# Optimization experiments

Hardware: AMD Instinct MI355X
Metric: run time of the kernel (lower is better)

The kernel has to match this reference:

```python
import jax, jax.numpy as jnp
import numpy as np

SEQ_LEN = 12
EMB = 64        # embedding_dim
H = 128         # dec_h_dim
MLP = 1024      # mlp_dim
Z = 32          # z_dim
ZX = MLP + Z    # 1056, width of cat([enc_h_feat, z])
B = 32768


def setup_inputs() -> dict:
    key = jax.random.key(0)
    ks = jax.random.split(key, 16)
    s = 0.05  # weight scale to keep the recurrence stable
    return {
        "last_pos": jax.random.normal(ks[0], (B, 2), jnp.float32),
        "last_pos_rel": jax.random.normal(ks[1], (B, 2), jnp.float32),
        "enc_h_feat": jax.random.normal(ks[2], (B, MLP), jnp.float32),
        "z": jax.random.normal(ks[3], (B, Z), jnp.float32),
        "seq_start_end": jnp.zeros((1, 2), jnp.int64),
        # LSTM params (PyTorch layout: gates ordered i,f,g,o along rows)
        "W_ih": jax.random.normal(ks[4], (4 * H, ZX + EMB), jnp.float32) * s,
        "W_hh": jax.random.normal(ks[5], (4 * H, H), jnp.float32) * s,
        "b_ih": jax.random.normal(ks[6], (4 * H,), jnp.float32) * s,
        "b_hh": jax.random.normal(ks[7], (4 * H,), jnp.float32) * s,
        # mlp: Linear(ZX->MLP), ReLU, Linear(MLP->H), ReLU
        "W1": jax.random.normal(ks[8], (MLP, ZX), jnp.float32) * s,
        "b1": jax.random.normal(ks[9], (MLP,), jnp.float32) * s,
        "W2": jax.random.normal(ks[10], (H, MLP), jnp.float32) * s,
        "b2": jax.random.normal(ks[11], (H,), jnp.float32) * s,
        # spatial_embedding: Linear(2 -> EMB)
        "W_sp": jax.random.normal(ks[12], (EMB, 2), jnp.float32) * s,
        "b_sp": jax.random.normal(ks[13], (EMB,), jnp.float32) * s,
        # hidden2pos: Linear(H -> 2)
        "W_hp": jax.random.normal(ks[14], (2, H), jnp.float32) * s,
        "b_hp": jax.random.normal(ks[15], (2,), jnp.float32) * s,
    }


def _decode(last_pos, last_pos_rel, enc_h_feat, z,
            W_ih, W_hh, b_ih, b_hh, W1, b1, W2, b2, W_sp, b_sp, W_hp, b_hp):
    # initial decoder input from last relative position
    dec_inp = last_pos_rel @ W_sp.T + b_sp                     # [B, EMB]
    zx = jnp.concatenate([enc_h_feat, z], axis=1)              # [B, ZX]
    h = jax.nn.relu(jax.nn.relu(zx @ W1.T + b1) @ W2.T + b2)   # [B, H]
    c = jnp.zeros_like(h)
    # zx is constant across steps: precompute its gate contribution + biases
    W_zx, W_emb = W_ih[:, :ZX], W_ih[:, ZX:]
    zx_proj = zx @ W_zx.T + b_ih + b_hh                        # [B, 4H]

    def step(carry, _):
        h, c, last_pos, dec_inp = carry
        gates = zx_proj + dec_inp @ W_emb.T + h @ W_hh.T       # [B, 4H]
        i, f, g, o = jnp.split(gates, 4, axis=1)
        c = jax.nn.sigmoid(f) * c + jax.nn.sigmoid(i) * jnp.tanh(g)
        h = jax.nn.sigmoid(o) * jnp.tanh(c)
        rel_pos = h @ W_hp.T + b_hp                            # [B, 2]
        last_pos = rel_pos + last_pos
        dec_inp = rel_pos @ W_sp.T + b_sp
        return (h, c, last_pos, dec_inp), rel_pos

    _, pred = jax.lax.scan(step, (h, c, last_pos, dec_inp), None, length=SEQ_LEN)
    return pred  # [SEQ_LEN, B, 2]


def reference(last_pos, last_pos_rel, enc_h_feat, z, seq_start_end,
              W_ih, W_hh, b_ih, b_hh, W1, b1, W2, b2, W_sp, b_sp, W_hp, b_hp):
    # seq_start_end is unused by the original forward
    return _decode(last_pos, last_pos_rel, enc_h_feat, z,
                   W_ih, W_hh, b_ih, b_hh, W1, b1, W2, b2, W_sp, b_sp, W_hp, b_hp)
```

## Files before the change

### kernel.cpp

```cpp
#include <hip/hip_runtime.h>

#define BATCH   32768
#define SEQLEN  12
#define EMB     64
#define H       128
#define MLP     1024
#define Z       32
#define ZX      1056
#define KP      1088
#define NG      512

typedef _Float16 f16x8 __attribute__((ext_vector_type(8)));
typedef float    f32x4 __attribute__((ext_vector_type(4)));

#define S_WCAT_OFF   0u
#define S_W2H_OFF    3244032u
#define S_WHHF_OFF   3506176u
#define S_WC_OFF     3637248u
#define S_BIAS2_OFF  3641344u
#define S_T1_OFF     3643392u
#define S_GP_OFF     70752256u
#define S_H0_OFF     137861120u
#define B_WCAT_OFF   0u
#define B_W2H_OFF    3342336u
#define B_WHHF_OFF   3604480u
#define B_WC_OFF     3735552u
#define B_BIAS2_OFF  3739648u
#define B_T1_OFF     3741696u
#define B_GP_OFF     70850560u
#define B_H0_OFF     137959424u
#define B_ZX16_OFF   146348032u
#define B_TOTAL      217651200ull

__device__ __forceinline__ float sigf(float x) {
    return __builtin_amdgcn_rcpf(1.0f + __expf(-x));
}
__device__ __forceinline__ float tanhfast(float x) {
    return 2.0f * __builtin_amdgcn_rcpf(1.0f + __expf(-2.0f * x)) - 1.0f;
}

__device__ __forceinline__ void gload16(const void* g, void* l) {
    __builtin_amdgcn_global_load_lds(
        (const __attribute__((address_space(1))) unsigned int*)(unsigned long long)(uintptr_t)g,
        (__attribute__((address_space(3))) unsigned int*)(unsigned int)(uintptr_t)l,
        16, 0, 0);
}

__global__ __launch_bounds__(256) void prep_kernel(
    const float* __restrict__ W_ih, const float* __restrict__ W_hh_in,
    const float* __restrict__ b_ih, const float* __restrict__ b_hh,
    const float* __restrict__ W1,   const float* __restrict__ W2,
    const float* __restrict__ W_sp, const float* __restrict__ b_sp,
    const float* __restrict__ W_hp, int cs,
    _Float16* __restrict__ wcat, _Float16* __restrict__ w2h,
    _Float16* __restrict__ whhf, float* __restrict__ wc, float* __restrict__ bias2)
{
    const int bid = blockIdx.x;
    const int tid = threadIdx.x;
    if (bid < 1536) {
        const float* src = (bid < 1024) ? (W1 + (size_t)bid * ZX)
                                        : (W_ih + (size_t)(bid - 1024) * 1120);
        _Float16* dst = wcat + (size_t)bid * cs;
        for (int k = tid; k < cs; k += 256)
            dst[k] = (k < ZX) ? (_Float16)src[k] : (_Float16)0.f;
    } else if (bid < 1664) {
        const int n = bid - 1536;
        for (int k = tid; k < MLP; k += 256)
            w2h[n * MLP + k] = (_Float16)W2[n * MLP + k];
    } else if (bid < 1920) {
        const int n = (bid - 1664) * 2 + (tid >> 7);
        const int k = tid & 127;
        float wc0 = 0.f, wc1 = 0.f;
        for (int e = 0; e < EMB; ++e) {
            const float we = W_ih[(size_t)n * 1120 + ZX + e];
            wc0 += we * W_sp[e * 2];
            wc1 += we * W_sp[e * 2 + 1];
        }
        whhf[n * H + k] = (_Float16)(W_hh_in[n * H + k] + wc0 * W_hp[k] + wc1 * W_hp[H + k]);
    } else {
        const int t = (bid - 1920) * 256 + tid;
        if (t < 1024) {
            const int n = t >> 1, j = t & 1;
            float s = 0.f;
            for (int e = 0; e < EMB; ++e)
                s += W_ih[(size_t)n * 1120 + ZX + e] * W_sp[e * 2 + j];
            wc[t] = s;
        } else if (t < 1536) {
            const int n = t - 1024;
            float s = b_ih[n] + b_hh[n];
            for (int e = 0; e < EMB; ++e)
                s += W_ih[(size_t)n * 1120 + ZX + e] * b_sp[e];
            bias2[n] = s;
        }
    }
}

__global__ __launch_bounds__(256) void zxcast_kernel(
    const float* __restrict__ enc, const float* __restrict__ zin,
    _Float16* __restrict__ zx16)
{
    const int gid = blockIdx.x * 256 + threadIdx.x;
    if (gid < 4194304) {
        const int row = gid >> 7, cw = gid & 127;
        const float4* s = (const float4*)(enc + (size_t)row * MLP + cw * 8);
        const float4 f0 = s[0], f1 = s[1];
        f16x8 v = {(_Float16)f0.x, (_Float16)f0.y, (_Float16)f0.z, (_Float16)f0.w,
                   (_Float16)f1.x, (_Float16)f1.y, (_Float16)f1.z, (_Float16)f1.w};
        *(f16x8*)(zx16 + (size_t)row * KP + cw * 8) = v;
    } else if (gid < 4325376) {
        const int g2 = gid - 4194304;
        const int row = g2 >> 2, cw = g2 & 3;
        const float4* s = (const float4*)(zin + (size_t)row * Z + cw * 8);
        const float4 f0 = s[0], f1 = s[1];
        f16x8 v = {(_Float16)f0.x, (_Float16)f0.y, (_Float16)f0.z, (_Float16)f0.w,
                   (_Float16)f1.x, (_Float16)f1.y, (_Float16)f1.z, (_Float16)f1.w};
        *(f16x8*)(zx16 + (size_t)row * KP + MLP + cw * 8) = v;
    } else {
        const int g2 = gid - 4325376;
        const int row = g2 >> 2, cw = g2 & 3;
        f16x8 v = {};
        *(f16x8*)(zx16 + (size_t)row * KP + ZX + cw * 8) = v;
    }
}

__global__ __launch_bounds__(256) void gemm1_big_kernel(
    const _Float16* __restrict__ zx16, const _Float16* __restrict__ wcat,
    const float* __restrict__ bias1, const float* __restrict__ bias2g,
    _Float16* __restrict__ t1, float* __restrict__ gperm)
{
    __shared__ _Float16 s_a[128 * 64];
    __shared__ _Float16 s_b[128 * 64];

    const int tid = threadIdx.x;
    const int b = blockIdx.x;
    const int x = b & 7, s = b >> 3;
    const int mt = x * 32 + s / 12;
    const int bn = s % 12;
    const int m0 = mt * 128;

    const int lane = tid & 63, wv = tid >> 6;
    const int wm = wv >> 1, wn = wv & 1;
    const int l15 = lane & 15, q = lane >> 4;

    const int rowS = tid >> 3;
    const int chS  = (tid & 7) ^ ((tid >> 3) & 7);

    f32x4 acc[4][4] = {};

    for (int kt = 0; kt < 17; ++kt) {
        __syncthreads();
        #pragma unroll
        for (int i = 0; i < 4; ++i)
            gload16(zx16 + (size_t)(m0 + i * 32 + rowS) * KP + kt * 64 + chS * 8,
                    s_a + i * 2048 + wv * 512);
        #pragma unroll
        for (int i = 0; i < 4; ++i)
            gload16(wcat + (size_t)(bn * 128 + i * 32 + rowS) * KP + kt * 64 + chS * 8,
                    s_b + i * 2048 + wv * 512);
        __syncthreads();

        #pragma unroll
        for (int kt2 = 0; kt2 < 2; ++kt2) {
            f16x8 af[4];
            #pragma unroll
            for (int im = 0; im < 4; ++im) {
                const int row = wm * 64 + im * 16 + l15;
                const int ph  = (kt2 * 4 + q) ^ (l15 & 7);
                af[im] = *(const f16x8*)(s_a + row * 64 + ph * 8);
            }
            #pragma unroll
            for (int in_ = 0; in_ < 4; ++in_) {
                const int row = wn * 64 + in_ * 16 + l15;
                const int ph  = (kt2 * 4 + q) ^ (l15 & 7);
                const f16x8 bf = *(const f16x8*)(s_b + row * 64 + ph * 8);
                #pragma unroll
                for (int im = 0; im < 4; ++im)
                    acc[im][in_] = __builtin_amdgcn_mfma_f32_16x16x32_f16(af[im], bf, acc[im][in_], 0, 0, 0);
            }
        }
    }

    if (bn < 8) {
        #pragma unroll
        for (int im = 0; im < 4; ++im)
            #pragma unroll
            for (int in_ = 0; in_ < 4; ++in_) {
                const int n = bn * 128 + wn * 64 + in_ * 16 + l15;
                const float bb = bias1[n];
                #pragma unroll
                for (int r = 0; r < 4; ++r) {
                    const int m = m0 + wm * 64 + im * 16 + q * 4 + r;
                    float v = acc[im][in_][r] + bb;
                    v = v > 0.f ? v : 0.f;
                    t1[(size_t)m * MLP + n] = (_Float16)v;
                }
            }
    } else {
        #pragma unroll
        for (int im = 0; im < 4; ++im)
            #pragma unroll
            for (int in_ = 0; in_ < 4; ++in_) {
                const int n = (bn - 8) * 128 + wn * 64 + in_ * 16 + l15;
                const float bb = bias2g[n];
                const int m4 = (m0 + wm * 64 + im * 16 + q * 4) >> 2;
                float4 v;
                v.x = acc[im][in_][0] + bb;
                v.y = acc[im][in_][1] + bb;
                v.z = acc[im][in_][2] + bb;
                v.w = acc[im][in_][3] + bb;
                *(float4*)(gperm + ((size_t)m4 * NG + n) * 4) = v;
            }
    }
}

__global__ __launch_bounds__(256) void gemm1_small_kernel(
    const float* __restrict__ enc, const float* __restrict__ zin,
    const _Float16* __restrict__ wcat,
    const float* __restrict__ bias1, const float* __restrict__ bias2g,
    _Float16* __restrict__ t1, float* __restrict__ gperm)
{
    __shared__ float    s_a[128 * 32];
    __shared__ _Float16 s_b[128 * 32];

    const int tid = threadIdx.x;
    const int b = blockIdx.x;
    const int x = b & 7, s = b >> 3;
    const int mt = x * 32 + s / 12;
    const int bn = s % 12;
    const int m0 = mt * 128;

    const int lane = tid & 63, wv = tid >> 6;
    const int wm = wv >> 1, wn = wv & 1;
    const int l15 = lane & 15, q = lane >> 4;

    const int rowA = tid >> 3;
    const int chA  = (tid & 7) ^ ((tid >> 3) & 7);
    const int rowB = tid >> 2;
    const int chB  = (tid & 3) ^ ((tid >> 3) & 3);

    const int ca0 = (2 * q) ^ (l15 & 7);
    const int cb  = q ^ ((l15 >> 1) & 3);

    f32x4 acc[4][4] = {};

    for (int kt = 0; kt < 33; ++kt) {
        const float* abase;
        size_t astride;
        if (kt < 32) { abase = enc + (size_t)m0 * MLP + kt * 32; astride = MLP; }
        else         { abase = zin + (size_t)m0 * Z;             astride = Z;   }

        __syncthreads();
        #pragma unroll
        for (int i = 0; i < 4; ++i)
            gload16(abase + (size_t)(i * 32 + rowA) * astride + chA * 4,
                    s_a + i * 1024 + wv * 256);
        #pragma unroll
        for (int i = 0; i < 2; ++i)
            gload16(wcat + (size_t)(bn * 128 + i * 64 + rowB) * ZX + kt * 32 + chB * 8,
                    s_b + i * 2048 + wv * 512);
        __syncthreads();

        f16x8 af[4];
        #pragma unroll
        for (int im = 0; im < 4; ++im) {
            const float* ap = s_a + (wm * 64 + im * 16 + l15) * 32;
            const float4 f0 = *(const float4*)(ap + ca0 * 4);
            const float4 f1 = *(const float4*)(ap + (ca0 ^ 1) * 4);
            af[im] = f16x8{(_Float16)f0.x, (_Float16)f0.y, (_Float16)f0.z, (_Float16)f0.w,
                           (_Float16)f1.x, (_Float16)f1.y, (_Float16)f1.z, (_Float16)f1.w};
        }
        #pragma unroll
        for (int in_ = 0; in_ < 4; ++in_) {
            const f16x8 bf = *(const f16x8*)(s_b + (wn * 64 + in_ * 16 + l15) * 32 + cb * 8);
            #pragma unroll
            for (int im = 0; im < 4; ++im)
                acc[im][in_] = __builtin_amdgcn_mfma_f32_16x16x32_f16(af[im], bf, acc[im][in_], 0, 0, 0);
        }
    }

    if (bn < 8) {
        #pragma unroll
        for (int im = 0; im < 4; ++im)
            #pragma unroll
            for (int in_ = 0; in_ < 4; ++in_) {
                const int n = bn * 128 + wn * 64 + in_ * 16 + l15;
                const float bb = bias1[n];
                #pragma unroll
                for (int r = 0; r < 4; ++r) {
                    const int m = m0 + wm * 64 + im * 16 + q * 4 + r;
                    float v = acc[im][in_][r] + bb;
                    v = v > 0.f ? v : 0.f;
                    t1[(size_t)m * MLP + n] = (_Float16)v;
                }
            }
    } else {
        #pragma unroll
        for (int im = 0; im < 4; ++im)
            #pragma unroll
            for (int in_ = 0; in_ < 4; ++in_) {
                const int n = (bn - 8) * 128 + wn * 64 + in_ * 16 + l15;
                const float bb = bias2g[n];
                const int m4 = (m0 + wm * 64 + im * 16 + q * 4) >> 2;
                float4 v;
                v.x = acc[im][in_][0] + bb;
                v.y = acc[im][in_][1] + bb;
                v.z = acc[im][in_][2] + bb;
                v.w = acc[im][in_][3] + bb;
                *(float4*)(gperm + ((size_t)m4 * NG + n) * 4) = v;
            }
    }
}

__global__ __launch_bounds__(256) void gemm2_kernel(
    const _Float16* __restrict__ t1, const _Float16* __restrict__ w2h,
    const float* __restrict__ b2, _Float16* __restrict__ h0buf)
{
    __shared__ _Float16 s_a[64 * 32];
    __shared__ _Float16 s_b[128 * 32];

    const int tid = threadIdx.x;
    const int m0  = blockIdx.x * 64;
    const int lane = tid & 63, wv = tid >> 6;
    const int l15 = lane & 15, q = lane >> 4;

    const int rowS = tid >> 2;
    const int chS  = ((tid & 3) ^ (tid >> 2) ^ (tid >> 4)) & 3;
    const int phF  = (q ^ l15 ^ (l15 >> 2)) & 3;

    f32x4 acc[4][2] = {};

    for (int kt = 0; kt < 32; ++kt) {
        __syncthreads();
        gload16(t1 + (size_t)(m0 + rowS) * MLP + kt * 32 + chS * 8,
                s_a + wv * 512);
        #pragma unroll
        for (int i = 0; i < 2; ++i) {
            const int row = i * 64 + rowS;
            const int c   = ((tid & 3) ^ row ^ (row >> 2)) & 3;
            gload16(w2h + (size_t)row * MLP + kt * 32 + c * 8,
                    s_b + i * 2048 + wv * 512);
        }
        __syncthreads();

        f16x8 af[4];
        #pragma unroll
        for (int im = 0; im < 4; ++im)
            af[im] = *(const f16x8*)(s_a + (im * 16 + l15) * 32 + phF * 8);
        #pragma unroll
        for (int in_ = 0; in_ < 2; ++in_) {
            const f16x8 bf = *(const f16x8*)(s_b + (wv * 32 + in_ * 16 + l15) * 32 + phF * 8);
            #pragma unroll
            for (int im = 0; im < 4; ++im)
                acc[im][in_] = __builtin_amdgcn_mfma_f32_16x16x32_f16(af[im], bf, acc[im][in_], 0, 0, 0);
        }
    }

    #pragma unroll
    for (int im = 0; im < 4; ++im)
        #pragma unroll
        for (int in_ = 0; in_ < 2; ++in_) {
            const int n = wv * 32 + in_ * 16 + l15;
            const float bb = b2[n];
            #pragma unroll
            for (int r = 0; r < 4; ++r) {
                const int m = m0 + im * 16 + q * 4 + r;
                float v = acc[im][in_][r] + bb;
                v = v > 0.f ? v : 0.f;
                h0buf[(size_t)m * H + n] = (_Float16)v;
            }
        }
}

__global__ __launch_bounds__(512) void recur_kernel(
    const float* __restrict__ gperm, const _Float16* __restrict__ h0buf,
    const _Float16* __restrict__ whhf, const float* __restrict__ wc,
    const float* __restrict__ whp, const float* __restrict__ bhp,
    const float* __restrict__ lpr, float* __restrict__ out)
{
    __shared__ _Float16 s_whh[512 * 136];
    __shared__ _Float16 s_h[64 * 136];
    __shared__ float    s_p[128];
    __shared__ float    s_wc[1024];
    __shared__ float    s_whp[256];
    __shared__ float    s_bhp[2];

    const int tid = threadIdx.x;
    const int m0  = blockIdx.x * 64;
    const int lane = tid & 63, w = tid >> 6;
    const int l15 = lane & 15, q = lane >> 4;

    #pragma unroll
    for (int i = 0; i < 16; ++i) {
        const int cid = tid + i * 512;
        const int row = cid >> 4, ch = cid & 15;
        *(uint4*)(s_whh + row * 136 + ch * 8) = *(const uint4*)(whhf + row * H + ch * 8);
    }
    if (tid < 256) *(float4*)(s_wc + tid * 4)  = *(const float4*)(wc + tid * 4);
    if (tid < 64)  *(float4*)(s_whp + tid * 4) = *(const float4*)(whp + tid * 4);
    if (tid < 2)   s_bhp[tid] = bhp[tid];
    if (tid < 128) s_p[tid] = lpr[(size_t)m0 * 2 + tid];
    {
        const int row = tid >> 3, ch = tid & 7;
        *(uint4*)(s_h + row * 136 + ch * 16)     = *(const uint4*)(h0buf + (size_t)(m0 + row) * H + ch * 16);
        *(uint4*)(s_h + row * 136 + ch * 16 + 8) = *(const uint4*)(h0buf + (size_t)(m0 + row) * H + ch * 16 + 8);
    }

    f32x4 gb[4][4];
    #pragma unroll
    for (int im = 0; im < 4; ++im) {
        const int m4 = (m0 >> 2) + im * 4 + q;
        #pragma unroll
        for (int g = 0; g < 4; ++g) {
            const float4 v = *(const float4*)(gperm + ((size_t)m4 * NG + g * H + w * 16 + l15) * 4);
            gb[im][g] = f32x4{v.x, v.y, v.z, v.w};
        }
    }

    f32x4 cst[4] = {};

    __syncthreads();

    {
        const int part = tid & 3;
        const int j    = (tid >> 2) & 1;
        const int row  = tid >> 3;
        float sum = 0.f;
        #pragma unroll
        for (int u = 0; u < 4; ++u) {
            const f16x8 hv = *(const f16x8*)(s_h + row * 136 + part * 32 + u * 8);
            const float4* wp = (const float4*)(s_whp + j * H + part * 32 + u * 8);
            const float4 w0 = wp[0], w1 = wp[1];
            sum += (float)hv[0] * w0.x + (float)hv[1] * w0.y + (float)hv[2] * w0.z + (float)hv[3] * w0.w
                 + (float)hv[4] * w1.x + (float)hv[5] * w1.y + (float)hv[6] * w1.z + (float)hv[7] * w1.w;
        }
        sum += __shfl_down(sum, 2, 64);
        sum += __shfl_down(sum, 1, 64);
        if (part == 0) s_p[row * 2 + j] -= sum;
    }
    __syncthreads();

    float wc0[4], wc1[4], cg[4];
    #pragma unroll
    for (int g = 0; g < 4; ++g) {
        const int n = g * H + w * 16 + l15;
        wc0[g] = s_wc[n * 2];
        wc1[g] = s_wc[n * 2 + 1];
        cg[g]  = wc0[g] * s_bhp[0] + wc1[g] * s_bhp[1];
    }
    #pragma unroll
    for (int im = 0; im < 4; ++im)
        #pragma unroll
        for (int r = 0; r < 4; ++r) {
            const int mrow = im * 16 + q * 4 + r;
            const float pa = s_p[mrow * 2], pb = s_p[mrow * 2 + 1];
            #pragma unroll
            for (int g = 0; g < 4; ++g)
                gb[im][g][r] += pa * wc0[g] + pb * wc1[g];
        }

    for (int t = 0; t < SEQLEN; ++t) {
        f32x4 acc[4][4];
        #pragma unroll
        for (int kt = 0; kt < 4; ++kt) {
            f16x8 af[4];
            #pragma unroll
            for (int im = 0; im < 4; ++im)
                af[im] = *(const f16x8*)(s_h + (im * 16 + l15) * 136 + kt * 32 + q * 8);
            #pragma unroll
            for (int g = 0; g < 4; ++g) {
                const f16x8 bf = *(const f16x8*)(s_whh + (g * H + w * 16 + l15) * 136 + kt * 32 + q * 8);
                #pragma unroll
                for (int im = 0; im < 4; ++im)
                    acc[im][g] = __builtin_amdgcn_mfma_f32_16x16x32_f16(
                        af[im], bf, (kt == 0) ? gb[im][g] : acc[im][g], 0, 0, 0);
            }
        }
        __syncthreads();

        #pragma unroll
        for (int im = 0; im < 4; ++im) {
            #pragma unroll
            for (int r = 0; r < 4; ++r) {
                const int mrow = im * 16 + q * 4 + r;
                const float cc = sigf(acc[im][1][r]) * cst[im][r]
                               + sigf(acc[im][0][r]) * tanhfast(acc[im][2][r]);
                cst[im][r] = cc;
                const float hh = sigf(acc[im][3][r]) * tanhfast(cc);
                s_h[mrow * 136 + w * 16 + l15] = (_Float16)hh;
            }
        }
        if (t == 0) {
            #pragma unroll
            for (int im = 0; im < 4; ++im)
                #pragma unroll
                for (int r = 0; r < 4; ++r) {
                    const int mrow = im * 16 + q * 4 + r;
                    const float pa = s_p[mrow * 2], pb = s_p[mrow * 2 + 1];
                    #pragma unroll
                    for (int g = 0; g < 4; ++g)
                        gb[im][g][r] += cg[g] - (pa * wc0[g] + pb * wc1[g]);
                }
        }
        __syncthreads();

        {
            const int part = tid & 3;
            const int j    = (tid >> 2) & 1;
            const int row  = tid >> 3;
            float sum = 0.f;
            #pragma unroll
            for (int u = 0; u < 4; ++u) {
                const f16x8 hv = *(const f16x8*)(s_h + row * 136 + part * 32 + u * 8);
                const float4* wp = (const float4*)(s_whp + j * H + part * 32 + u * 8);
                const float4 w0 = wp[0], w1 = wp[1];
                sum += (float)hv[0] * w0.x + (float)hv[1] * w0.y + (float)hv[2] * w0.z + (float)hv[3] * w0.w
                     + (float)hv[4] * w1.x + (float)hv[5] * w1.y + (float)hv[6] * w1.z + (float)hv[7] * w1.w;
            }
            sum += __shfl_down(sum, 2, 64);
            sum += __shfl_down(sum, 1, 64);
            if (part == 0)
                out[(size_t)t * (BATCH * 2) + (size_t)(m0 + row) * 2 + j] = sum + s_bhp[j];
        }
    }
}

extern "C" void kernel_launch(void* const* d_in, const int* in_sizes, int n_in,
                              void* d_out, int out_size, void* d_ws, size_t ws_size,
                              hipStream_t stream)
{
    const float* last_pos_rel = (const float*)d_in[1];
    const float* enc          = (const float*)d_in[2];
    const float* zin          = (const float*)d_in[3];
    const float* W_ih         = (const float*)d_in[5];
    const float* W_hh         = (const float*)d_in[6];
    const float* b_ih         = (const float*)d_in[7];
    const float* b_hh         = (const float*)d_in[8];
    const float* W1           = (const float*)d_in[9];
    const float* b1           = (const float*)d_in[10];
    const float* W2           = (const float*)d_in[11];
    const float* b2           = (const float*)d_in[12];
    const float* W_sp         = (const float*)d_in[13];
    const float* b_sp         = (const float*)d_in[14];
    const float* W_hp         = (const float*)d_in[15];
    const float* b_hp         = (const float*)d_in[16];
    float* out = (float*)d_out;

    char* ws = (char*)d_ws;
    const bool big = (ws_size >= B_TOTAL);

    _Float16* wcat  = (_Float16*)(ws + (big ? B_WCAT_OFF  : S_WCAT_OFF));
    _Float16* w2h   = (_Float16*)(ws + (big ? B_W2H_OFF   : S_W2H_OFF));
    _Float16* whhf  = (_Float16*)(ws + (big ? B_WHHF_OFF  : S_WHHF_OFF));
    float*    wc    = (float*)(ws + (big ? B_WC_OFF    : S_WC_OFF));
    float*    bias2 = (float*)(ws + (big ? B_BIAS2_OFF : S_BIAS2_OFF));
    _Float16* t1    = (_Float16*)(ws + (big ? B_T1_OFF : S_T1_OFF));
    float*    gperm = (float*)(ws + (big ? B_GP_OFF : S_GP_OFF));
    _Float16* h0b   = (_Float16*)(ws + (big ? B_H0_OFF : S_H0_OFF));
    _Float16* zx16  = (_Float16*)(ws + B_ZX16_OFF);

    prep_kernel<<<dim3(1926), 256, 0, stream>>>(W_ih, W_hh, b_ih, b_hh, W1, W2, W_sp, b_sp,
                                                W_hp, big ? KP : ZX, wcat, w2h, whhf, wc, bias2);
    if (big) {
        zxcast_kernel<<<dim3(17408), 256, 0, stream>>>(enc, zin, zx16);
        gemm1_big_kernel<<<dim3(3072), 256, 0, stream>>>(zx16, wcat, b1, bias2, t1, gperm);
    } else {
        gemm1_small_kernel<<<dim3(3072), 256, 0, stream>>>(enc, zin, wcat, b1, bias2, t1, gperm);
    }
    gemm2_kernel<<<dim3(512), 256, 0, stream>>>(t1, w2h, b2, h0b);
    recur_kernel<<<dim3(512), 512, 0, stream>>>(gperm, h0b, whhf, wc, W_hp, b_hp,
                                                last_pos_rel, out);
}
```

Baseline: 530.6 us.

## Keep recurrent weights in registers and vectorize weight conversion in prep

The recurrence kernel no longer stages the 512x128 fp16 W_hh matrix in shared memory. Each wave instead loads its own MFMA B-fragments into registers once, and launch bounds request two blocks per CU. This cuts LDS use from about 150KB to about 25KB, which permits more resident blocks and removes the per-step LDS reads of weights, at the cost of 64 extra VGPRs per thread. The prep kernel's fp32-to-fp16 weight conversion is also vectorized to 8-wide loads and stores.

```diff
diff --git a/kernel.cpp b/kernel.cpp
--- a/kernel.cpp
+++ b/kernel.cpp
@@ -61,12 +61,26 @@
         const float* src = (bid < 1024) ? (W1 + (size_t)bid * ZX)
                                         : (W_ih + (size_t)(bid - 1024) * 1120);
         _Float16* dst = wcat + (size_t)bid * cs;
-        for (int k = tid; k < cs; k += 256)
-            dst[k] = (k < ZX) ? (_Float16)src[k] : (_Float16)0.f;
+        const int nch = cs >> 3;
+        for (int c = tid; c < nch; c += 256) {
+            f16x8 v = {};
+            if (c < 132) {
+                const float4 f0 = *(const float4*)(src + c * 8);
+                const float4 f1 = *(const float4*)(src + c * 8 + 4);
+                v = f16x8{(_Float16)f0.x, (_Float16)f0.y, (_Float16)f0.z, (_Float16)f0.w,
+                          (_Float16)f1.x, (_Float16)f1.y, (_Float16)f1.z, (_Float16)f1.w};
+            }
+            *(f16x8*)(dst + c * 8) = v;
+        }
     } else if (bid < 1664) {
         const int n = bid - 1536;
-        for (int k = tid; k < MLP; k += 256)
-            w2h[n * MLP + k] = (_Float16)W2[n * MLP + k];
+        for (int c = tid; c < 128; c += 256) {
+            const float4 f0 = *(const float4*)(W2 + (size_t)n * MLP + c * 8);
+            const float4 f1 = *(const float4*)(W2 + (size_t)n * MLP + c * 8 + 4);
+            f16x8 v = {(_Float16)f0.x, (_Float16)f0.y, (_Float16)f0.z, (_Float16)f0.w,
+                       (_Float16)f1.x, (_Float16)f1.y, (_Float16)f1.z, (_Float16)f1.w};
+            *(f16x8*)(w2h + (size_t)n * MLP + c * 8) = v;
+        }
     } else if (bid < 1920) {
         const int n = (bid - 1664) * 2 + (tid >> 7);
         const int k = tid & 127;
@@ -371,13 +385,12 @@
         }
 }
 
-__global__ __launch_bounds__(512) void recur_kernel(
+__global__ __launch_bounds__(512, 2) void recur_kernel(
     const float* __restrict__ gperm, const _Float16* __restrict__ h0buf,
     const _Float16* __restrict__ whhf, const float* __restrict__ wc,
     const float* __restrict__ whp, const float* __restrict__ bhp,
     const float* __restrict__ lpr, float* __restrict__ out)
 {
-    __shared__ _Float16 s_whh[512 * 136];
     __shared__ _Float16 s_h[64 * 136];
     __shared__ float    s_p[128];
     __shared__ float    s_wc[1024];
@@ -389,12 +402,13 @@
     const int lane = tid & 63, w = tid >> 6;
     const int l15 = lane & 15, q = lane >> 4;
 
+    f16x8 bfr[4][4];
     #pragma unroll
-    for (int i = 0; i < 16; ++i) {
-        const int cid = tid + i * 512;
-        const int row = cid >> 4, ch = cid & 15;
-        *(uint4*)(s_whh + row * 136 + ch * 8) = *(const uint4*)(whhf + row * H + ch * 8);
-    }
+    for (int g = 0; g < 4; ++g)
+        #pragma unroll
+        for (int kt = 0; kt < 4; ++kt)
+            bfr[g][kt] = *(const f16x8*)(whhf + (size_t)(g * H + w * 16 + l15) * H + kt * 32 + q * 8);
+
     if (tid < 256) *(float4*)(s_wc + tid * 4)  = *(const float4*)(wc + tid * 4);
     if (tid < 64)  *(float4*)(s_whp + tid * 4) = *(const float4*)(whp + tid * 4);
     if (tid < 2)   s_bhp[tid] = bhp[tid];
@@ -467,13 +481,11 @@
             for (int im = 0; im < 4; ++im)
                 af[im] = *(const f16x8*)(s_h + (im * 16 + l15) * 136 + kt * 32 + q * 8);
             #pragma unroll
-            for (int g = 0; g < 4; ++g) {
-                const f16x8 bf = *(const f16x8*)(s_whh + (g * H + w * 16 + l15) * 136 + kt * 32 + q * 8);
+            for (int g = 0; g < 4; ++g)
                 #pragma unroll
                 for (int im = 0; im < 4; ++im)
                     acc[im][g] = __builtin_amdgcn_mfma_f32_16x16x32_f16(
-                        af[im], bf, (kt == 0) ? gb[im][g] : acc[im][g], 0, 0, 0);
-            }
+                        af[im], bfr[g][kt], (kt == 0) ? gb[im][g] : acc[im][g], 0, 0, 0);
         }
         __syncthreads();
 
```

After: 573.8 us. 1.08x slower.
